# Performance work log

Measured on AMD Instinct MI355X. Metric: run time of the kernel, lower is better.

Reference implementation:

```python
import jax, jax.numpy as jnp
import numpy as np

T, B, F = 160, 640, 40          # time-major input [T, B, F]
H, PJ, L = 768, 256, 3          # nb_hidden, nb_proj, nb_layers
FORGET_BIAS = 1.0               # TF LSTMCell default


def _glorot(k, shape):
    std = (2.0 / (shape[0] + shape[1])) ** 0.5
    return jax.random.normal(k, shape, jnp.float32) * std


def setup_inputs() -> dict:
    key = jax.random.key(0)
    ks = jax.random.split(key, 7)
    x = jax.random.normal(ks[0], (T, B, F), jnp.float32)
    # layer 0: input dim F + proj state PJ; layers 1,2: input dim PJ + PJ
    W0 = _glorot(ks[1], (F + PJ, 4 * H)); b0 = jnp.zeros((4 * H,), jnp.float32)
    P0 = _glorot(ks[2], (H, PJ))
    W1 = _glorot(ks[3], (PJ + PJ, 4 * H)); b1 = jnp.zeros((4 * H,), jnp.float32)
    P1 = _glorot(ks[4], (H, PJ))
    W2 = _glorot(ks[5], (PJ + PJ, 4 * H)); b2 = jnp.zeros((4 * H,), jnp.float32)
    P2 = _glorot(ks[6], (H, PJ))
    return {"x": x, "W0": W0, "b0": b0, "P0": P0,
            "W1": W1, "b1": b1, "P1": P1,
            "W2": W2, "b2": b2, "P2": P2}


def _cell(xt, c, h, W, b, P):
    # TF LSTMCell with num_proj: gates on [x, m_prev]; gate order i, j, f, o.
    z = jnp.concatenate([xt, h], axis=-1) @ W + b            # [B, 4H]
    i, j, f, o = jnp.split(z, 4, axis=-1)
    c_new = jax.nn.sigmoid(f + FORGET_BIAS) * c + jax.nn.sigmoid(i) * jnp.tanh(j)
    m = jax.nn.sigmoid(o) * jnp.tanh(c_new)                  # [B, H]
    h_new = m @ P                                            # projected state [B, PJ]
    return c_new, h_new


def reference(x, W0, b0, P0, W1, b1, P1, W2, b2, P2):
    params = ((W0, b0, P0), (W1, b1, P1), (W2, b2, P2))
    Bd = x.shape[1]
    init = tuple((jnp.zeros((Bd, H), x.dtype), jnp.zeros((Bd, PJ), x.dtype))
                 for _ in range(L))

    def step(carry, xt):
        inp = xt
        new = []
        for (c, h), (W, b, P) in zip(carry, params):
            c, h = _cell(inp, c, h, W, b, P)
            new.append((c, h))
            inp = h
        return tuple(new), None

    carry, _ = jax.lax.scan(step, init, x)
    emb = carry[-1][1]                                       # last layer h at final step, [B, PJ]
    # tf.nn.l2_normalize
    return emb / jnp.sqrt(jnp.maximum(jnp.sum(emb * emb, axis=-1, keepdims=True), 1e-12))
```

## Files before the change

kernel.cpp:

```cpp
#include <hip/hip_runtime.h>
#include <hip/hip_cooperative_groups.h>

namespace cg = cooperative_groups;

#define Bdim 640
#define Hdim 768
#define PJdim 256
#define Tdim 160
#define NSTEP (Tdim + 2)

typedef _Float16 half8 __attribute__((ext_vector_type(8)));
typedef float floatx16 __attribute__((ext_vector_type(16)));

constexpr size_t HF_HALFS = 3ull * 5 * 16 * 4 * 512;
constexpr size_t MB_HALFS = 3ull * 5 * 48 * 4 * 512;
constexpr size_t XF_HALFS = 160ull * 5 * 4 * 4 * 512;
constexpr size_t WF_HALFS = 36ull * 32 * 8 * 512;
constexpr size_t PF_HALFS = 3ull * 4 * 48 * 2 * 512;
constexpr size_t HF_OFF  = 0;
constexpr size_t MB_OFF  = HF_HALFS * 2;
constexpr size_t XF_OFF  = MB_OFF + MB_HALFS * 2;
constexpr size_t WF_OFF  = XF_OFF + XF_HALFS * 2;
constexpr size_t PF_OFF  = WF_OFF + WF_HALFS * 2;
constexpr size_t CFB_OFF = PF_OFF + PF_HALFS * 2;
constexpr size_t CFB_BYTES = 180ull * 512 * 16 * 4;

__device__ __forceinline__ float sigm(float v) { return 1.0f / (1.0f + __expf(-v)); }
__device__ __forceinline__ float tanh_fast(float v) { return 2.0f / (1.0f + __expf(-2.0f * v)) - 1.0f; }

__global__ void repack_kernel(const float* __restrict__ x,
                              const float* __restrict__ W0, const float* __restrict__ W1,
                              const float* __restrict__ W2, const float* __restrict__ P0,
                              const float* __restrict__ P1, const float* __restrict__ P2,
                              _Float16* __restrict__ Wfrag, _Float16* __restrict__ Pfrag,
                              _Float16* __restrict__ xF)
{
    size_t idx = (size_t)blockIdx.x * 256 + threadIdx.x;
    if (idx < WF_HALFS) {
        int slab = (int)(idx >> 17);
        int l = slab / 12, ht = slab % 12;
        int r = (int)(idx & 131071);
        int kc = r >> 12;
        int wvp = (r >> 9) & 7;
        int u = r & 511;
        int lane = u >> 3, e = u & 7;
        int g = wvp >> 1, hh = wvp & 1;
        int col = g * Hdim + ht * 64 + hh * 32 + (lane & 31);
        int a = kc * 16 + (lane >> 5) * 8 + e;
        float v = 0.0f;
        if (l == 0) {
            if (a < 256)      v = W0[(size_t)(40 + a) * 3072 + col];
            else if (a < 296) v = W0[(size_t)(a - 256) * 3072 + col];
        } else if (a < 512) {
            const float* W = (l == 1) ? W1 : W2;
            v = W[(size_t)a * 3072 + col];
        }
        Wfrag[idx] = (_Float16)v;
    } else if (idx < WF_HALFS + PF_HALFS) {
        size_t i = idx - WF_HALFS;
        int l = (int)(i / 196608);
        int r = (int)(i % 196608);
        int cq = r / 49152;
        int r2 = r % 49152;
        int kc = r2 / 1024;
        int cgp = (r2 >> 9) & 1;
        int u = r2 & 511;
        int lane = u >> 3, e = u & 7;
        int pj = cq * 64 + cgp * 32 + (lane & 31);
        int k = kc * 16 + (lane >> 5) * 8 + e;
        const float* P = (l == 0) ? P0 : (l == 1) ? P1 : P2;
        Pfrag[i] = (_Float16)P[(size_t)k * PJdim + pj];
    } else if (idx < WF_HALFS + PF_HALFS + XF_HALFS) {
        size_t i = idx - WF_HALFS - PF_HALFS;
        int t = (int)(i / 40960);
        int r = (int)(i % 40960);
        int bt2 = r / 8192;
        int r2 = r % 8192;
        int kcx = r2 / 2048;
        int rt = (r2 >> 9) & 3;
        int u = r2 & 511;
        int lane = u >> 3, e = u & 7;
        int row = bt2 * 128 + rt * 32 + (lane & 31);
        int xcol = kcx * 16 + (lane >> 5) * 8 + e;
        float v = (xcol < 40) ? x[((size_t)t * Bdim + row) * 40 + xcol] : 0.0f;
        xF[i] = (_Float16)v;
    }
}

template <int G>
__device__ __forceinline__ void gate_gemm(const uint4* const (&gs)[8], const half8 (&Breg)[32],
                                          floatx16 (&acc)[4], _Float16* Abuf, int tid, int lane)
{
    {
        uint4 v0 = gs[0][tid], v1 = gs[0][tid + 512];
        uint4* d = (uint4*)Abuf;
        d[tid] = v0; d[tid + 512] = v1;
        __syncthreads();
    }
#pragma unroll
    for (int g = 0; g < G; ++g) {
        uint4 p0, p1;
        const bool pf = (g + 1 < G);
        if (pf) { p0 = gs[g + 1][tid]; p1 = gs[g + 1][tid + 512]; }
        const _Float16* base = Abuf + (g & 1) * 8192;
#pragma unroll
        for (int c4 = 0; c4 < 4; ++c4) {
#pragma unroll
            for (int rt = 0; rt < 4; ++rt) {
                half8 a = *(const half8*)(base + (c4 * 4 + rt) * 512 + lane * 8);
                acc[rt] = __builtin_amdgcn_mfma_f32_32x32x16_f16(a, Breg[g * 4 + c4], acc[rt], 0, 0, 0);
            }
        }
        if (pf) {
            uint4* d = (uint4*)(Abuf + ((g + 1) & 1) * 8192);
            d[tid] = p0; d[tid + 512] = p1;
        }
        __syncthreads();
    }
}

__device__ __forceinline__ void proj_gemm(const uint4* const (&gs)[12], const half8 (&Preg)[48],
                                          floatx16& pacc, _Float16* Abuf, int tid, int lane, int rh)
{
    {
        uint4 v0 = gs[0][tid], v1 = gs[0][tid + 512];
        uint4* d = (uint4*)Abuf;
        d[tid] = v0; d[tid + 512] = v1;
        __syncthreads();
    }
#pragma unroll
    for (int g = 0; g < 12; ++g) {
        uint4 p0, p1;
        const bool pf = (g + 1 < 12);
        if (pf) { p0 = gs[g + 1][tid]; p1 = gs[g + 1][tid + 512]; }
        const _Float16* base = Abuf + (g & 1) * 8192;
#pragma unroll
        for (int c4 = 0; c4 < 4; ++c4) {
            half8 a = *(const half8*)(base + (c4 * 4 + rh) * 512 + lane * 8);
            pacc = __builtin_amdgcn_mfma_f32_32x32x16_f16(a, Preg[g * 4 + c4], pacc, 0, 0, 0);
        }
        if (pf) {
            uint4* d = (uint4*)(Abuf + ((g + 1) & 1) * 8192);
            d[tid] = p0; d[tid + 512] = p1;
        }
        __syncthreads();
    }
}

__device__ __forceinline__ void gate_run(int l, int ht, int bt2, int t,
                                         const half8 (&Breg)[32], float bv, float (&c)[8][2],
                                         const _Float16* __restrict__ hF,
                                         const _Float16* __restrict__ xF,
                                         _Float16* __restrict__ mbufF,
                                         char* smem, int tid)
{
    const int wv = tid >> 6, lane = tid & 63;
    const int g = wv >> 1, hh = wv & 1;
    _Float16* Abuf = (_Float16*)smem;

    floatx16 acc[4];
#pragma unroll
    for (int rt = 0; rt < 4; ++rt)
#pragma unroll
        for (int e = 0; e < 16; ++e) acc[rt][e] = 0.f;

    const uint4* gs[8];
    if (l == 0) {
        const _Float16* own = hF + (size_t)bt2 * 32768;
#pragma unroll
        for (int g2 = 0; g2 < 4; ++g2) gs[g2] = (const uint4*)(own + g2 * 8192);
        gs[4] = (const uint4*)(xF + ((size_t)t * 5 + bt2) * 8192);
        gs[5] = gs[6] = gs[7] = gs[4];
        gate_gemm<5>(gs, Breg, acc, Abuf, tid, lane);
    } else {
        const _Float16* lo = hF + ((size_t)(l - 1) * 5 + bt2) * 32768;
        const _Float16* hi = hF + ((size_t)l * 5 + bt2) * 32768;
#pragma unroll
        for (int g2 = 0; g2 < 4; ++g2) {
            gs[g2] = (const uint4*)(lo + g2 * 8192);
            gs[4 + g2] = (const uint4*)(hi + g2 * 8192);
        }
        gate_gemm<8>(gs, Breg, acc, Abuf, tid, lane);
    }

    float* zst = (float*)smem;
    _Float16* Mlds = (_Float16*)(smem + 16384);
    const int gcol = g * 64 + hh * 32 + (lane & 31);
    const int trow = tid >> 5, uu = tid & 31, hc0 = 2 * uu;
#pragma unroll
    for (int p = 0; p < 8; ++p) {
#pragma unroll
        for (int rr = 0; rr < 8; ++rr) {
            int r16 = (rr & 3) + ((rr >> 2) << 3) + ((lane >> 5) << 2);
            zst[r16 * 256 + gcol] = acc[p >> 1][(p & 1) * 8 + rr] + bv;
        }
        __syncthreads();
        unsigned pk = 0;
#pragma unroll
        for (int jj = 0; jj < 2; ++jj) {
            int hc = hc0 + jj;
            float zi = zst[trow * 256 + hc];
            float zj = zst[trow * 256 + 64 + hc];
            float zf = zst[trow * 256 + 128 + hc];
            float zo = zst[trow * 256 + 192 + hc];
            float cn = sigm(zf) * c[p][jj] + sigm(zi) * tanh_fast(zj);
            c[p][jj] = cn;
            _Float16 mh = (_Float16)(sigm(zo) * tanh_fast(cn));
            unsigned short us = *(unsigned short*)&mh;
            pk |= ((unsigned)us) << (16 * jj);
        }
        {
            int f = (p >> 1) * 4 + (hc0 >> 4);
            int lane32 = (p & 1) * 16 + trow + 32 * ((hc0 >> 3) & 1);
            *(unsigned*)(Mlds + f * 512 + lane32 * 8 + (hc0 & 7)) = pk;
        }
        __syncthreads();
    }
    {
        int f = tid >> 5, o = (tid & 31) * 16;
        uint4 w0 = *(const uint4*)(Mlds + f * 512 + o);
        uint4 w1 = *(const uint4*)(Mlds + f * 512 + o + 8);
        _Float16* dst = mbufF + ((((size_t)l * 5 + bt2) * 48 + ht * 4 + (f & 3)) * 4 + (f >> 2)) * 512 + o;
        *(uint4*)dst = w0;
        *(uint4*)(dst + 8) = w1;
    }
}

__device__ __forceinline__ void proj_run(int l, int cq, int bt2, const half8 (&Preg)[48],
                                         const _Float16* __restrict__ mbufF,
                                         _Float16* __restrict__ hF,
                                         char* smem, int tid)
{
    const int wv = tid >> 6, lane = tid & 63;
    const int rh = wv >> 1, cgp = wv & 1;
    _Float16* Abuf = (_Float16*)smem;

    floatx16 pacc;
#pragma unroll
    for (int e = 0; e < 16; ++e) pacc[e] = 0.f;

    const _Float16* mslice = mbufF + ((size_t)l * 5 + bt2) * 98304;
    const uint4* gs[12];
#pragma unroll
    for (int g2 = 0; g2 < 12; ++g2) gs[g2] = (const uint4*)(mslice + g2 * 8192);
    proj_gemm(gs, Preg, pacc, Abuf, tid, lane, rh);

    _Float16* Hlds = (_Float16*)smem;
    const int col32 = lane & 31;
    const int fH = (cgp * 2 + (col32 >> 4)) * 4 + rh;
    const int lane32 = 32 * ((col32 >> 3) & 1);
    const int e0 = col32 & 7;
#pragma unroll
    for (int q = 0; q < 4; ++q)
#pragma unroll
        for (int i = 0; i < 4; ++i) {
            int row32 = i + 8 * q + 4 * (lane >> 5);
            Hlds[fH * 512 + (row32 + lane32) * 8 + e0] = (_Float16)pacc[q * 4 + i];
        }
    __syncthreads();
    {
        int f = tid >> 5, o = (tid & 31) * 16;
        uint4 w0 = *(const uint4*)(Hlds + f * 512 + o);
        uint4 w1 = *(const uint4*)(Hlds + f * 512 + o + 8);
        _Float16* dst = hF + ((((size_t)l * 5 + bt2) * 16 + cq * 4 + (f >> 2)) * 4 + (f & 3)) * 512 + o;
        *(uint4*)dst = w0;
        *(uint4*)(dst + 8) = w1;
    }
    __syncthreads();
}

__device__ __forceinline__ void finalize_row(const _Float16* __restrict__ hF,
                                             float* __restrict__ out, int row, int lane)
{
    int bt2 = row >> 7, rt = (row >> 5) & 3, r32 = row & 31;
    int kcH = lane >> 2;
    int l32 = r32 + 32 * ((lane >> 1) & 1);
    int e0 = (lane & 1) * 4;
    const _Float16* p = hF + ((((size_t)10 + bt2) * 16 + kcH) * 4 + rt) * 512 + l32 * 8 + e0;
    float v0 = (float)p[0], v1 = (float)p[1], v2 = (float)p[2], v3 = (float)p[3];
    float ss = v0 * v0 + v1 * v1 + v2 * v2 + v3 * v3;
#pragma unroll
    for (int o = 32; o > 0; o >>= 1) ss += __shfl_xor(ss, o, 64);
    float rs = rsqrtf(fmaxf(ss, 1e-12f));
    float4 o4;
    o4.x = v0 * rs; o4.y = v1 * rs; o4.z = v2 * rs; o4.w = v3 * rs;
    *(float4*)(out + (size_t)row * PJdim + lane * 4) = o4;
}

__global__ __launch_bounds__(512, 1)
void lstm_persist(const _Float16* __restrict__ xF, const _Float16* __restrict__ Wfrag,
                  const _Float16* __restrict__ Pfrag,
                  const float* __restrict__ bias0, const float* __restrict__ bias1,
                  const float* __restrict__ bias2,
                  _Float16* __restrict__ hF, _Float16* __restrict__ mbufF,
                  float* __restrict__ out)
{
    cg::grid_group grid = cg::this_grid();
    __shared__ __align__(16) char smem[32768];
    const int tid = threadIdx.x, bid = blockIdx.x;
    const int wv = tid >> 6, lane = tid & 63;
    const int xc = bid & 7, j = bid >> 3;

    int role = 0, l = 0, ht = 0, bt2 = 0, cq = 0;
    if (j < 24) {
        int grp = xc + 8 * (j / 12);
        if (grp < 15) { role = 1; l = grp / 5; bt2 = grp % 5; ht = j % 12; }
    } else {
        int grp = (j < 28) ? xc : xc + 8;
        if (grp < 15) { role = 2; l = grp / 5; bt2 = grp % 5; cq = (j < 28) ? (j - 24) : (j - 28); }
    }

    if (role == 1) {
        half8 Breg[32];
        const _Float16* wslab = Wfrag + (size_t)(l * 12 + ht) * 131072;
        const int nkc = (l == 0) ? 20 : 32;
#pragma unroll
        for (int kc = 0; kc < 32; ++kc)
            if (kc < nkc) Breg[kc] = *(const half8*)(wslab + (kc * 8 + wv) * 512 + lane * 8);
        const float* bias = (l == 0) ? bias0 : (l == 1) ? bias1 : bias2;
        const int g = wv >> 1, hh = wv & 1;
        const float bv = bias[g * Hdim + ht * 64 + hh * 32 + (lane & 31)] + ((g == 2) ? 1.0f : 0.0f);
        float c[8][2];
#pragma unroll
        for (int p = 0; p < 8; ++p) { c[p][0] = 0.f; c[p][1] = 0.f; }
        for (int s = 0; s < NSTEP; ++s) {
            const int t = s - l;
            if (t >= 0 && t < Tdim)
                gate_run(l, ht, bt2, t, Breg, bv, c, hF, xF, mbufF, smem, tid);
            grid.sync();
            grid.sync();
        }
    } else if (role == 2) {
        half8 Preg[48];
        const _Float16* pslab = Pfrag + ((size_t)l * 4 + cq) * 49152;
#pragma unroll
        for (int kc = 0; kc < 48; ++kc)
            Preg[kc] = *(const half8*)(pslab + (kc * 2 + (wv & 1)) * 512 + lane * 8);
        for (int s = 0; s < NSTEP; ++s) {
            grid.sync();
            const int t = s - l;
            if (t >= 0 && t < Tdim)
                proj_run(l, cq, bt2, Preg, mbufF, hF, smem, tid);
            grid.sync();
        }
    } else {
        for (int s = 0; s < NSTEP; ++s) { grid.sync(); grid.sync(); }
    }

    if (bid < 80) finalize_row(hF, out, bid * 8 + wv, lane);
}

__global__ __launch_bounds__(512, 1)
void gate_fb(const _Float16* __restrict__ xF, const _Float16* __restrict__ Wfrag,
             const float* __restrict__ bias0, const float* __restrict__ bias1,
             const float* __restrict__ bias2,
             _Float16* __restrict__ hF, _Float16* __restrict__ mbufF,
             float* __restrict__ cfb, int s)
{
    __shared__ __align__(16) char smem[32768];
    const int tid = threadIdx.x, bid = blockIdx.x;
    const int l = bid / 60, r = bid % 60, ht = r / 5, bt2 = r % 5;
    const int t = s - l;
    if (t < 0 || t >= Tdim) return;
    const int wv = tid >> 6, lane = tid & 63;
    half8 Breg[32];
    const _Float16* wslab = Wfrag + (size_t)(l * 12 + ht) * 131072;
    const int nkc = (l == 0) ? 20 : 32;
#pragma unroll
    for (int kc = 0; kc < 32; ++kc)
        if (kc < nkc) Breg[kc] = *(const half8*)(wslab + (kc * 8 + wv) * 512 + lane * 8);
    const float* bias = (l == 0) ? bias0 : (l == 1) ? bias1 : bias2;
    const int g = wv >> 1, hh = wv & 1;
    const float bv = bias[g * Hdim + ht * 64 + hh * 32 + (lane & 31)] + ((g == 2) ? 1.0f : 0.0f);
    float c[8][2];
    size_t cb = ((size_t)bid * 512 + tid) * 16;
#pragma unroll
    for (int p = 0; p < 8; ++p) { c[p][0] = cfb[cb + p * 2]; c[p][1] = cfb[cb + p * 2 + 1]; }
    gate_run(l, ht, bt2, t, Breg, bv, c, hF, xF, mbufF, smem, tid);
#pragma unroll
    for (int p = 0; p < 8; ++p) { cfb[cb + p * 2] = c[p][0]; cfb[cb + p * 2 + 1] = c[p][1]; }
}

__global__ __launch_bounds__(512, 1)
void proj_fb(const _Float16* __restrict__ Pfrag, const _Float16* __restrict__ mbufF,
             _Float16* __restrict__ hF, int s)
{
    __shared__ __align__(16) char smem[32768];
    const int tid = threadIdx.x, bid = blockIdx.x;
    const int l = bid / 20, r = bid % 20, cq = r / 5, bt2 = r % 5;
    const int t = s - l;
    if (t < 0 || t >= Tdim) return;
    const int wv = tid >> 6, lane = tid & 63;
    half8 Preg[48];
    const _Float16* pslab = Pfrag + ((size_t)l * 4 + cq) * 49152;
#pragma unroll
    for (int kc = 0; kc < 48; ++kc)
        Preg[kc] = *(const half8*)(pslab + (kc * 2 + (wv & 1)) * 512 + lane * 8);
    proj_run(l, cq, bt2, Preg, mbufF, hF, smem, tid);
}

__global__ __launch_bounds__(512, 1)
void fin_fb(const _Float16* __restrict__ hF, float* __restrict__ out)
{
    finalize_row(hF, out, blockIdx.x * 8 + (threadIdx.x >> 6), threadIdx.x & 63);
}

extern "C" void kernel_launch(void* const* d_in, const int* in_sizes, int n_in,
                              void* d_out, int out_size, void* d_ws, size_t ws_size,
                              hipStream_t stream)
{
    (void)in_sizes; (void)n_in; (void)out_size; (void)ws_size;
    const float* x  = (const float*)d_in[0];
    const float* W0 = (const float*)d_in[1];
    const float* b0 = (const float*)d_in[2];
    const float* P0 = (const float*)d_in[3];
    const float* W1 = (const float*)d_in[4];
    const float* b1 = (const float*)d_in[5];
    const float* P1 = (const float*)d_in[6];
    const float* W2 = (const float*)d_in[7];
    const float* b2 = (const float*)d_in[8];
    const float* P2 = (const float*)d_in[9];

    char* ws = (char*)d_ws;
    _Float16* hF    = (_Float16*)(ws + HF_OFF);
    _Float16* mbufF = (_Float16*)(ws + MB_OFF);
    _Float16* xF    = (_Float16*)(ws + XF_OFF);
    _Float16* Wfrag = (_Float16*)(ws + WF_OFF);
    _Float16* Pfrag = (_Float16*)(ws + PF_OFF);
    float*    cfb   = (float*)(ws + CFB_OFF);
    float*    outp  = (float*)d_out;

    hipMemsetAsync(hF, 0, HF_HALFS * 2, stream);
    hipMemsetAsync(cfb, 0, CFB_BYTES, stream);

    {
        constexpr size_t total = WF_HALFS + PF_HALFS + XF_HALFS;
        int grid = (int)((total + 255) / 256);
        repack_kernel<<<grid, 256, 0, stream>>>(x, W0, W1, W2, P0, P1, P2, Wfrag, Pfrag, xF);
    }

    int occ = 0;
    hipError_t oe = hipOccupancyMaxActiveBlocksPerMultiprocessor(&occ, lstm_persist, 512, 0);
    bool coop = (oe == hipSuccess && occ >= 1);
    if (coop) {
        void* args[] = { (void*)&xF, (void*)&Wfrag, (void*)&Pfrag,
                         (void*)&b0, (void*)&b1, (void*)&b2,
                         (void*)&hF, (void*)&mbufF, (void*)&outp };
        hipError_t le = hipLaunchCooperativeKernel((const void*)lstm_persist,
                                                   dim3(256), dim3(512), args, 0, stream);
        if (le != hipSuccess) { (void)hipGetLastError(); coop = false; }
    }
    if (!coop) {
        for (int s = 0; s < NSTEP; ++s) {
            gate_fb<<<180, 512, 0, stream>>>(xF, Wfrag, b0, b1, b2, hF, mbufF, cfb, s);
            proj_fb<<<60, 512, 0, stream>>>(Pfrag, mbufF, hF, s);
        }
        fin_fb<<<80, 512, 0, stream>>>(hF, outp);
    }
}
```

Before: 5.939 ms.

## Replace grid-wide syncs with per-slot atomic counters and double-buffered state

The persistent LSTM kernel's two grid.sync calls per wavefront step are replaced by fine-grained dataflow synchronization. Gate and projection blocks spin on per-slot acquire/release atomic counters, waiting only on the tiles they depend on. The h and m buffers are double-buffered by time parity so producers can run ahead without overwriting data still being read. This removes the global barrier cost and lets layers pipeline more loosely, at the cost of spin-wait polling, extra workspace and more complex ordering that could deadlock or race if the dependencies are wrong.

After: 5.334 ms. -10.2%, faster.

```diff
diff --git a/kernel.cpp b/kernel.cpp
--- a/kernel.cpp
+++ b/kernel.cpp
@@ -12,21 +12,30 @@
 typedef _Float16 half8 __attribute__((ext_vector_type(8)));
 typedef float floatx16 __attribute__((ext_vector_type(16)));
 
-constexpr size_t HF_HALFS = 3ull * 5 * 16 * 4 * 512;
-constexpr size_t MB_HALFS = 3ull * 5 * 48 * 4 * 512;
+#define HFP 491520u
+#define MBP 1474560u
+constexpr size_t CNT_OFF = 0;
+constexpr size_t HF_OFF  = 16384;
+constexpr size_t MB_OFF  = HF_OFF + 2ull * HFP * 2;
+constexpr size_t XF_OFF  = MB_OFF + 2ull * MBP * 2;
 constexpr size_t XF_HALFS = 160ull * 5 * 4 * 4 * 512;
+constexpr size_t WF_OFF  = XF_OFF + XF_HALFS * 2;
 constexpr size_t WF_HALFS = 36ull * 32 * 8 * 512;
+constexpr size_t PF_OFF  = WF_OFF + WF_HALFS * 2;
 constexpr size_t PF_HALFS = 3ull * 4 * 48 * 2 * 512;
-constexpr size_t HF_OFF  = 0;
-constexpr size_t MB_OFF  = HF_HALFS * 2;
-constexpr size_t XF_OFF  = MB_OFF + MB_HALFS * 2;
-constexpr size_t WF_OFF  = XF_OFF + XF_HALFS * 2;
-constexpr size_t PF_OFF  = WF_OFF + WF_HALFS * 2;
 constexpr size_t CFB_OFF = PF_OFF + PF_HALFS * 2;
 constexpr size_t CFB_BYTES = 180ull * 512 * 16 * 4;
 
 __device__ __forceinline__ float sigm(float v) { return 1.0f / (1.0f + __expf(-v)); }
 __device__ __forceinline__ float tanh_fast(float v) { return 2.0f / (1.0f + __expf(-2.0f * v)) - 1.0f; }
+
+__device__ __forceinline__ void waitGE(int* p, int tgt) {
+    while (__hip_atomic_load(p, __ATOMIC_ACQUIRE, __HIP_MEMORY_SCOPE_AGENT) < tgt)
+        __builtin_amdgcn_s_sleep(1);
+}
+__device__ __forceinline__ void signal1(int* p) {
+    __hip_atomic_fetch_add(p, 1, __ATOMIC_RELEASE, __HIP_MEMORY_SCOPE_AGENT);
+}
 
 __global__ void repack_kernel(const float* __restrict__ x,
                               const float* __restrict__ W0, const float* __restrict__ W1,
@@ -147,11 +156,12 @@
     }
 }
 
-__device__ __forceinline__ void gate_run(int l, int ht, int bt2, int t,
+__device__ __forceinline__ void gate_run(int l,
+                                         const _Float16* __restrict__ hOwnSlab,
+                                         const _Float16* __restrict__ hBelSlab,
+                                         const _Float16* __restrict__ xGran,
+                                         _Float16* __restrict__ mslab,
                                          const half8 (&Breg)[32], float bv, float (&c)[8][2],
-                                         const _Float16* __restrict__ hF,
-                                         const _Float16* __restrict__ xF,
-                                         _Float16* __restrict__ mbufF,
                                          char* smem, int tid)
 {
     const int wv = tid >> 6, lane = tid & 63;
@@ -166,19 +176,16 @@
 
     const uint4* gs[8];
     if (l == 0) {
-        const _Float16* own = hF + (size_t)bt2 * 32768;
-#pragma unroll
-        for (int g2 = 0; g2 < 4; ++g2) gs[g2] = (const uint4*)(own + g2 * 8192);
-        gs[4] = (const uint4*)(xF + ((size_t)t * 5 + bt2) * 8192);
+#pragma unroll
+        for (int g2 = 0; g2 < 4; ++g2) gs[g2] = (const uint4*)(hOwnSlab + g2 * 8192);
+        gs[4] = (const uint4*)xGran;
         gs[5] = gs[6] = gs[7] = gs[4];
         gate_gemm<5>(gs, Breg, acc, Abuf, tid, lane);
     } else {
-        const _Float16* lo = hF + ((size_t)(l - 1) * 5 + bt2) * 32768;
-        const _Float16* hi = hF + ((size_t)l * 5 + bt2) * 32768;
 #pragma unroll
         for (int g2 = 0; g2 < 4; ++g2) {
-            gs[g2] = (const uint4*)(lo + g2 * 8192);
-            gs[4 + g2] = (const uint4*)(hi + g2 * 8192);
+            gs[g2] = (const uint4*)(hBelSlab + g2 * 8192);
+            gs[4 + g2] = (const uint4*)(hOwnSlab + g2 * 8192);
         }
         gate_gemm<8>(gs, Breg, acc, Abuf, tid, lane);
     }
@@ -220,16 +227,15 @@
         int f = tid >> 5, o = (tid & 31) * 16;
         uint4 w0 = *(const uint4*)(Mlds + f * 512 + o);
         uint4 w1 = *(const uint4*)(Mlds + f * 512 + o + 8);
-        _Float16* dst = mbufF + ((((size_t)l * 5 + bt2) * 48 + ht * 4 + (f & 3)) * 4 + (f >> 2)) * 512 + o;
+        _Float16* dst = mslab + (size_t)(f & 3) * 2048 + (f >> 2) * 512 + o;
         *(uint4*)dst = w0;
         *(uint4*)(dst + 8) = w1;
     }
 }
 
-__device__ __forceinline__ void proj_run(int l, int cq, int bt2, const half8 (&Preg)[48],
-                                         const _Float16* __restrict__ mbufF,
-                                         _Float16* __restrict__ hF,
-                                         char* smem, int tid)
+__device__ __forceinline__ void proj_run(const _Float16* __restrict__ mslice,
+                                         _Float16* __restrict__ hdstBase,
+                                         const half8 (&Preg)[48], char* smem, int tid)
 {
     const int wv = tid >> 6, lane = tid & 63;
     const int rh = wv >> 1, cgp = wv & 1;
@@ -239,7 +245,6 @@
 #pragma unroll
     for (int e = 0; e < 16; ++e) pacc[e] = 0.f;
 
-    const _Float16* mslice = mbufF + ((size_t)l * 5 + bt2) * 98304;
     const uint4* gs[12];
 #pragma unroll
     for (int g2 = 0; g2 < 12; ++g2) gs[g2] = (const uint4*)(mslice + g2 * 8192);
@@ -262,21 +267,21 @@
         int f = tid >> 5, o = (tid & 31) * 16;
         uint4 w0 = *(const uint4*)(Hlds + f * 512 + o);
         uint4 w1 = *(const uint4*)(Hlds + f * 512 + o + 8);
-        _Float16* dst = hF + ((((size_t)l * 5 + bt2) * 16 + cq * 4 + (f >> 2)) * 4 + (f & 3)) * 512 + o;
+        _Float16* dst = hdstBase + (size_t)(f >> 2) * 2048 + (f & 3) * 512 + o;
         *(uint4*)dst = w0;
         *(uint4*)(dst + 8) = w1;
     }
     __syncthreads();
 }
 
-__device__ __forceinline__ void finalize_row(const _Float16* __restrict__ hF,
+__device__ __forceinline__ void finalize_row(const _Float16* __restrict__ hPar1,
                                              float* __restrict__ out, int row, int lane)
 {
     int bt2 = row >> 7, rt = (row >> 5) & 3, r32 = row & 31;
     int kcH = lane >> 2;
     int l32 = r32 + 32 * ((lane >> 1) & 1);
     int e0 = (lane & 1) * 4;
-    const _Float16* p = hF + ((((size_t)10 + bt2) * 16 + kcH) * 4 + rt) * 512 + l32 * 8 + e0;
+    const _Float16* p = hPar1 + ((((size_t)10 + bt2) * 16 + kcH) * 4 + rt) * 512 + l32 * 8 + e0;
     float v0 = (float)p[0], v1 = (float)p[1], v2 = (float)p[2], v3 = (float)p[3];
     float ss = v0 * v0 + v1 * v1 + v2 * v2 + v3 * v3;
 #pragma unroll
@@ -293,9 +298,8 @@
                   const float* __restrict__ bias0, const float* __restrict__ bias1,
                   const float* __restrict__ bias2,
                   _Float16* __restrict__ hF, _Float16* __restrict__ mbufF,
-                  float* __restrict__ out)
-{
-    cg::grid_group grid = cg::this_grid();
+                  int* __restrict__ cnt, float* __restrict__ out)
+{
     __shared__ __align__(16) char smem[32768];
     const int tid = threadIdx.x, bid = blockIdx.x;
     const int wv = tid >> 6, lane = tid & 63;
@@ -309,6 +313,7 @@
         int grp = (j < 28) ? xc : xc + 8;
         if (grp < 15) { role = 2; l = grp / 5; bt2 = grp % 5; cq = (j < 28) ? (j - 24) : (j - 28); }
     }
+    const int slot = l * 5 + bt2;
 
     if (role == 1) {
         half8 Breg[32];
@@ -323,12 +328,25 @@
         float c[8][2];
 #pragma unroll
         for (int p = 0; p < 8; ++p) { c[p][0] = 0.f; c[p][1] = 0.f; }
-        for (int s = 0; s < NSTEP; ++s) {
-            const int t = s - l;
-            if (t >= 0 && t < Tdim)
-                gate_run(l, ht, bt2, t, Breg, bv, c, hF, xF, mbufF, smem, tid);
-            grid.sync();
-            grid.sync();
+
+        int* mC = cnt + ((size_t)slot * 12 + ht) * 16;
+        const _Float16* hOwnSlabs = hF;
+        for (int t = 0; t < Tdim; ++t) {
+            if (tid == 0) {
+                if (t > 0)
+                    for (int q = 0; q < 4; ++q) waitGE(cnt + (180 + (size_t)slot * 4 + q) * 16, t);
+                if (l > 0)
+                    for (int q = 0; q < 4; ++q) waitGE(cnt + (180 + (size_t)(slot - 5) * 4 + q) * 16, t + 1);
+            }
+            __syncthreads();
+            const _Float16* hOwn = hOwnSlabs + (size_t)((t + 1) & 1) * HFP + (size_t)slot * 32768;
+            const _Float16* hBel = (l > 0) ? hOwnSlabs + (size_t)(t & 1) * HFP + (size_t)(slot - 5) * 32768
+                                           : nullptr;
+            const _Float16* xG = xF + ((size_t)t * 5 + bt2) * 8192;
+            _Float16* mslab = mbufF + (size_t)(t & 1) * MBP + ((size_t)slot * 48 + ht * 4) * 2048;
+            gate_run(l, hOwn, hBel, xG, mslab, Breg, bv, c, smem, tid);
+            __syncthreads();
+            if (tid == 0) signal1(mC);
         }
     } else if (role == 2) {
         half8 Preg[48];
@@ -336,18 +354,29 @@
 #pragma unroll
         for (int kc = 0; kc < 48; ++kc)
             Preg[kc] = *(const half8*)(pslab + (kc * 2 + (wv & 1)) * 512 + lane * 8);
-        for (int s = 0; s < NSTEP; ++s) {
-            grid.sync();
-            const int t = s - l;
-            if (t >= 0 && t < Tdim)
-                proj_run(l, cq, bt2, Preg, mbufF, hF, smem, tid);
-            grid.sync();
-        }
-    } else {
-        for (int s = 0; s < NSTEP; ++s) { grid.sync(); grid.sync(); }
-    }
-
-    if (bid < 80) finalize_row(hF, out, bid * 8 + wv, lane);
+
+        int* pC = cnt + (180 + (size_t)slot * 4 + cq) * 16;
+        for (int t = 0; t < Tdim; ++t) {
+            if (tid == 0) {
+                for (int h2 = 0; h2 < 12; ++h2) waitGE(cnt + ((size_t)slot * 12 + h2) * 16, t + 1);
+                if (l < 2 && t >= 2)
+                    for (int h2 = 0; h2 < 12; ++h2) waitGE(cnt + ((size_t)(slot + 5) * 12 + h2) * 16, t - 1);
+            }
+            __syncthreads();
+            const _Float16* mslice = mbufF + (size_t)(t & 1) * MBP + (size_t)slot * 98304;
+            _Float16* hdst = hF + (size_t)(t & 1) * HFP + ((size_t)slot * 16 + cq * 4) * 2048;
+            proj_run(mslice, hdst, Preg, smem, tid);
+            if (tid == 0) signal1(pC);
+        }
+        if (l == 2) {
+            if (tid == 0)
+                for (int q = 0; q < 4; ++q) waitGE(cnt + (180 + (size_t)slot * 4 + q) * 16, Tdim);
+            __syncthreads();
+#pragma unroll
+            for (int i = 0; i < 4; ++i)
+                finalize_row(hF + HFP, out, bt2 * 128 + cq * 32 + wv * 4 + i, lane);
+        }
+    }
 }
 
 __global__ __launch_bounds__(512, 1)
@@ -359,10 +388,11 @@
 {
     __shared__ __align__(16) char smem[32768];
     const int tid = threadIdx.x, bid = blockIdx.x;
-    const int l = bid / 60, r = bid % 60, ht = r / 5, bt2 = r % 5;
+    const int l = bid / 60, r = bid % 60, ht = r / 12 == 0 ? r % 12 : r % 12, bt2 = r / 12;
     const int t = s - l;
     if (t < 0 || t >= Tdim) return;
     const int wv = tid >> 6, lane = tid & 63;
+    const int slot = l * 5 + bt2;
     half8 Breg[32];
     const _Float16* wslab = Wfrag + (size_t)(l * 12 + ht) * 131072;
     const int nkc = (l == 0) ? 20 : 32;
@@ -376,7 +406,11 @@
     size_t cb = ((size_t)bid * 512 + tid) * 16;
 #pragma unroll
     for (int p = 0; p < 8; ++p) { c[p][0] = cfb[cb + p * 2]; c[p][1] = cfb[cb + p * 2 + 1]; }
-    gate_run(l, ht, bt2, t, Breg, bv, c, hF, xF, mbufF, smem, tid);
+    const _Float16* hOwn = hF + (size_t)((t + 1) & 1) * HFP + (size_t)slot * 32768;
+    const _Float16* hBel = (l > 0) ? hF + (size_t)(t & 1) * HFP + (size_t)(slot - 5) * 32768 : nullptr;
+    const _Float16* xG = xF + ((size_t)t * 5 + bt2) * 8192;
+    _Float16* mslab = mbufF + (size_t)(t & 1) * MBP + ((size_t)slot * 48 + ht * 4) * 2048;
+    gate_run(l, hOwn, hBel, xG, mslab, Breg, bv, c, smem, tid);
 #pragma unroll
     for (int p = 0; p < 8; ++p) { cfb[cb + p * 2] = c[p][0]; cfb[cb + p * 2 + 1] = c[p][1]; }
 }
@@ -391,18 +425,21 @@
     const int t = s - l;
     if (t < 0 || t >= Tdim) return;
     const int wv = tid >> 6, lane = tid & 63;
+    const int slot = l * 5 + bt2;
     half8 Preg[48];
     const _Float16* pslab = Pfrag + ((size_t)l * 4 + cq) * 49152;
 #pragma unroll
     for (int kc = 0; kc < 48; ++kc)
         Preg[kc] = *(const half8*)(pslab + (kc * 2 + (wv & 1)) * 512 + lane * 8);
-    proj_run(l, cq, bt2, Preg, mbufF, hF, smem, tid);
+    const _Float16* mslice = mbufF + (size_t)(t & 1) * MBP + (size_t)slot * 98304;
+    _Float16* hdst = hF + (size_t)(t & 1) * HFP + ((size_t)slot * 16 + cq * 4) * 2048;
+    proj_run(mslice, hdst, Preg, smem, tid);
 }
 
 __global__ __launch_bounds__(512, 1)
 void fin_fb(const _Float16* __restrict__ hF, float* __restrict__ out)
 {
-    finalize_row(hF, out, blockIdx.x * 8 + (threadIdx.x >> 6), threadIdx.x & 63);
+    finalize_row(hF + HFP, out, blockIdx.x * 8 + (threadIdx.x >> 6), threadIdx.x & 63);
 }
 
 extern "C" void kernel_launch(void* const* d_in, const int* in_sizes, int n_in,
@@ -422,6 +459,7 @@
     const float* P2 = (const float*)d_in[9];
 
     char* ws = (char*)d_ws;
+    int*      cnt   = (int*)(ws + CNT_OFF);
     _Float16* hF    = (_Float16*)(ws + HF_OFF);
     _Float16* mbufF = (_Float16*)(ws + MB_OFF);
     _Float16* xF    = (_Float16*)(ws + XF_OFF);
@@ -430,7 +468,7 @@
     float*    cfb   = (float*)(ws + CFB_OFF);
     float*    outp  = (float*)d_out;
 
-    hipMemsetAsync(hF, 0, HF_HALFS * 2, stream);
+    hipMemsetAsync(ws, 0, HF_OFF + 2ull * HFP * 2, stream);
     hipMemsetAsync(cfb, 0, CFB_BYTES, stream);
 
     {
@@ -445,7 +483,7 @@
     if (coop) {
         void* args[] = { (void*)&xF, (void*)&Wfrag, (void*)&Pfrag,
                          (void*)&b0, (void*)&b1, (void*)&b2,
-                         (void*)&hF, (void*)&mbufF, (void*)&outp };
+                         (void*)&hF, (void*)&mbufF, (void*)&cnt, (void*)&outp };
         hipError_t le = hipLaunchCooperativeKernel((const void*)lstm_persist,
                                                    dim3(256), dim3(512), args, 0, stream);
         if (le != hipSuccess) { (void)hipGetLastError(); coop = false; }
```
